# Performance work log

Hardware: AMD Instinct MI355X
Metric: run time of the kernel (lower is better)

Reference implementation:

```python
import jax, jax.numpy as jnp
import numpy as np

S = 72
IMG_W, IMG_H = 640, 360
STRIDE = 32
FMAP_H, FMAP_W = IMG_H // STRIDE, IMG_W // STRIDE  # 11, 20
N_OFFSETS = S
N_STRIPS = S - 1
ANGLES = np.array([15.0, 22.0, 30.0, 39.0, 49.0, 60.0, 72.0, 80.0, 90.0, 100.0, 108.0, 120.0, 131.0, 141.0, 150.0, 158.0, 165.0])
N_ANG = 17
N_PRED = 2 + 2 + 1 + N_OFFSETS  # 77
N_EDGE = FMAP_W + 2 * FMAP_H    # 42
N_PROP = N_ANG * N_EDGE         # 714
NMS_THRES = 15.0
BACKBONE_C = 512
CONV_C = 1024


def _make_anchors():
    anchor_ys = np.linspace(1.0, 0.0, N_OFFSETS)
    tan = np.tan(np.deg2rad(ANGLES))
    def side(origins):
        out = np.zeros((N_ANG, N_PRED, len(origins)), np.float32)
        for i, (sx, sy) in enumerate(origins):
            out[:, 2, i] = 1.0 - sy
            out[:, 3, i] = sx
            out[:, 5:, i] = (sx + (sy - anchor_ys)[None, :] / tan[:, None]) * IMG_W
        return out.reshape(N_ANG * N_PRED, len(origins))
    left = side([(0.0, y) for y in np.linspace(1.0, 0.0, FMAP_H)])
    right = side([(1.0, y) for y in np.linspace(1.0, 0.0, FMAP_H)])
    bottom = side([(x, 1.0) for x in np.linspace(1.0, 0.0, FMAP_W)])
    anchors = np.zeros((N_ANG * N_PRED, FMAP_H, FMAP_W), np.float32)
    anchors[:, :, 0] = left
    anchors[:, :, -1] = right
    anchors[:, -1, :] = bottom
    edge = np.concatenate([anchors[:, :, 0], anchors[:, :, -1], anchors[:, -1, :]], 1)  # [1309,42]
    anch_dim = edge.reshape(N_ANG, N_PRED, N_EDGE).transpose(2, 0, 1).reshape(N_PROP, N_PRED)
    return jnp.asarray(anchors), jnp.asarray(anch_dim)


def setup_inputs():
    key = jax.random.key(0)
    ks = jax.random.split(key, 4)
    B = 32
    feat = jax.random.normal(ks[0], (B, BACKBONE_C, FMAP_H, FMAP_W), jnp.float32)
    W_conv = jax.random.normal(ks[1], (CONV_C, BACKBONE_C), jnp.float32) * 0.02
    b_conv = jnp.zeros((CONV_C,), jnp.float32)
    W_cls = jax.random.normal(ks[2], (2 * N_ANG, CONV_C), jnp.float32) * 0.02
    b_cls = jnp.zeros((2 * N_ANG,), jnp.float32)
    W_reg = jax.random.normal(ks[3], (N_ANG * (N_OFFSETS + 1), CONV_C), jnp.float32) * 0.02
    b_reg = jnp.zeros((N_ANG * (N_OFFSETS + 1),), jnp.float32)
    anchors, anchors_anchor_dim = _make_anchors()
    return {"feat": feat, "W_conv": W_conv, "b_conv": b_conv, "W_cls": W_cls, "b_cls": b_cls,
            "W_reg": W_reg, "b_reg": b_reg, "anchors": anchors, "anchors_anchor_dim": anchors_anchor_dim}


def _proposals(feat, W_conv, b_conv, W_cls, b_cls, W_reg, b_reg, anchors):
    B = feat.shape[0]
    features = jnp.einsum('bchw,oc->bohw', feat, W_conv) + b_conv[None, :, None, None]
    cls_f = jnp.einsum('bchw,oc->bohw', features, W_cls) + b_cls[None, :, None, None]
    reg_f = jnp.einsum('bchw,oc->bohw', features, W_reg) + b_reg[None, :, None, None]
    anch = anchors.reshape(N_ANG, N_PRED, FMAP_H, FMAP_W)
    cls_r = cls_f.reshape(B, N_ANG, 2, FMAP_H, FMAP_W)
    reg_r = reg_f.reshape(B, N_ANG, N_OFFSETS + 1, FMAP_H, FMAP_W)
    # slots 0:2 <- cls logits (set), slots 2:4 <- anchor (copied), slots 4: <- anchor + reg
    mid = jnp.broadcast_to(anch[None, :, 2:4], (B, N_ANG, 2, FMAP_H, FMAP_W))
    tail = anch[None, :, 4:] + reg_r
    lane = jnp.concatenate([cls_r, mid, tail], axis=2)  # [B,17,77,h,w]
    # gather the three feature-map edges: left col, right col, bottom row
    edges = jnp.concatenate([lane[:, :, :, :, 0], lane[:, :, :, :, -1], lane[:, :, :, -1, :]], axis=3)  # [B,17,77,42]
    return edges.transpose(0, 3, 1, 2).reshape(B, N_PROP, N_PRED)  # [B,714,77]


def _nms_one(props, scores):
    # greedy line-NMS over proposals of one image, shapes static
    order = jnp.argsort(-scores)
    p = props[order]
    start = jnp.clip(jnp.round(p[:, 2] * N_STRIPS), 0.0, float(N_STRIPS))
    end = jnp.clip(start + p[:, 4] - 1.0, 0.0, float(N_STRIPS))
    xs = p[:, 5:]  # [N,72]
    s = jnp.maximum(start[:, None], start[None, :])
    e = jnp.minimum(end[:, None], end[None, :])
    idx = jnp.arange(N_OFFSETS, dtype=p.dtype)
    m = (idx[None, None, :] >= s[..., None]) & (idx[None, None, :] <= e[..., None])  # [N,N,72]
    diff = jnp.abs(xs[:, None, :] - xs[None, :, :])  # [N,N,72]
    cnt = e - s + 1.0
    dist = jnp.where(cnt > 0, jnp.sum(diff * m, -1) / jnp.maximum(cnt, 1.0), jnp.inf)
    sup = dist < NMS_THRES
    n = p.shape[0]
    pos = jnp.arange(n)
    def step(suppressed, i):
        keep_i = ~suppressed[i]
        suppressed = suppressed | (keep_i & sup[i] & (pos > i))
        return suppressed, keep_i
    _, keep_sorted = jax.lax.scan(step, jnp.zeros(n, bool), pos)
    return jnp.zeros(n, bool).at[order].set(keep_sorted)


def reference(feat, W_conv, b_conv, W_cls, b_cls, W_reg, b_reg, anchors, anchors_anchor_dim):
    proposals = _proposals(feat, W_conv, b_conv, W_cls, b_cls, W_reg, b_reg, anchors)
    scores = jax.nn.softmax(proposals[..., :2], axis=-1)[..., 1]  # [B,714]
    keep_mask = jax.lax.map(lambda pr: _nms_one(pr[0], pr[1]), (proposals, scores))  # [B,714]
    return proposals, keep_mask, scores
```

## Files before the change

kernel.cpp:

```cpp
#include <hip/hip_runtime.h>
#include <math.h>

#define NB     32
#define FH     11
#define FW     20
#define CIN    512
#define CMID   1024
#define NANG   17
#define NPREDD 77
#define NEDGE  42
#define NPROPP 714
#define NOFF   72
#define NCLS   34
#define NREGR  1241
#define N2PAD  1280
#define MTOT   1344
#define NSTRIPSF 71.0f
#define PADK   40

typedef unsigned long long u64;
typedef unsigned short ushortt;
typedef short s8v __attribute__((ext_vector_type(8)));
typedef ushortt u4v __attribute__((ext_vector_type(4)));
typedef float f4v __attribute__((ext_vector_type(4)));

__device__ inline ushortt f2bf(float f) {
    unsigned u = __float_as_uint(f);
    u += 0x7fffu + ((u >> 16) & 1u);
    return (ushortt)(u >> 16);
}
__device__ inline float bf2f(ushortt h) {
    return __uint_as_float(((unsigned)h) << 16);
}

__global__ __launch_bounds__(256) void k_prep(const float* __restrict__ feat,
                                              ushortt* __restrict__ A1hi,
                                              ushortt* __restrict__ A1lo,
                                              const float* __restrict__ Wconv,
                                              ushortt* __restrict__ B1h,
                                              ushortt* __restrict__ B1l,
                                              const float* __restrict__ Wcls,
                                              const float* __restrict__ Wreg,
                                              ushortt* __restrict__ B2h,
                                              ushortt* __restrict__ B2l)
{
    __shared__ unsigned T[32 * 221];
    int bid = blockIdx.x, tid = threadIdx.x;
    if (bid < 512) {
        int p0 = bid * 32;
        int b  = p0 >> 9;
        int c0 = p0 & 511;
        const float* fp = feat + (size_t)p0 * 220;
        for (int i = tid; i < 32 * 220; i += 256) {
            float v = fp[i];
            int pl = i / 220, off = i - pl * 220;
            ushortt hi = f2bf(v);
            ushortt lo = f2bf(v - bf2f(hi));
            T[pl * 221 + off] = ((unsigned)hi) | (((unsigned)lo) << 16);
        }
        __syncthreads();
        int cl = tid & 31;
        for (int e = tid >> 5; e < NEDGE; e += 8) {
            int hw = (e < FH) ? e * FW
                   : (e < 2 * FH) ? (e - FH) * FW + (FW - 1)
                   : (FH - 1) * FW + (e - 2 * FH);
            unsigned u = T[cl * 221 + hw];
            size_t o = (size_t)(b * NEDGE + e) * CIN + c0 + cl;
            A1hi[o] = (ushortt)(u & 0xffffu);
            A1lo[o] = (ushortt)(u >> 16);
        }
    } else if (bid < 1024) {
        int t = (bid - 512) * 256 + tid;
        float4 v = *(const float4*)(Wconv + (size_t)t * 4);
        float vf[4] = {v.x, v.y, v.z, v.w};
        u4v hv, lv;
#pragma unroll
        for (int j = 0; j < 4; ++j) {
            ushortt h = f2bf(vf[j]);
            hv[j] = h;
            lv[j] = f2bf(vf[j] - bf2f(h));
        }
        *(u4v*)(B1h + (size_t)t * 4) = hv;
        *(u4v*)(B1l + (size_t)t * 4) = lv;
    } else {
        int t = (bid - 1024) * 256 + tid;
        int row = t >> 8, col = (t & 255) * 4;
        float4 v = make_float4(0.f, 0.f, 0.f, 0.f);
        if (row < NCLS)              v = *(const float4*)(Wcls + (size_t)row * CMID + col);
        else if (row < NCLS + NREGR) v = *(const float4*)(Wreg + (size_t)(row - NCLS) * CMID + col);
        float vf[4] = {v.x, v.y, v.z, v.w};
        u4v hv, lv;
#pragma unroll
        for (int j = 0; j < 4; ++j) {
            ushortt h = f2bf(vf[j]);
            hv[j] = h;
            lv[j] = f2bf(vf[j] - bf2f(h));
        }
        *(u4v*)(B2h + (size_t)t * 4) = hv;
        *(u4v*)(B2l + (size_t)t * 4) = lv;
    }
}

#define GEMM_STEP(BUF)                                                               \
    {                                                                                \
        s8v ah[2], al[2], bh[2], bl[2];                                              \
        _Pragma("unroll")                                                            \
        for (int s = 0; s < 2; ++s) {                                                \
            ah[s] = *(const s8v*)&Ash[BUF][(wm + s * 16 + l15) * PADK + quad * 8];   \
            al[s] = *(const s8v*)&Asl[BUF][(wm + s * 16 + l15) * PADK + quad * 8];   \
            bh[s] = *(const s8v*)&Bsh[BUF][(wn + s * 16 + l15) * PADK + quad * 8];   \
            bl[s] = *(const s8v*)&Bsl[BUF][(wn + s * 16 + l15) * PADK + quad * 8];   \
        }                                                                            \
        _Pragma("unroll")                                                            \
        for (int sm = 0; sm < 2; ++sm)                                               \
            _Pragma("unroll")                                                        \
            for (int sn = 0; sn < 2; ++sn) {                                         \
                acc[sm][sn] = __builtin_amdgcn_mfma_f32_16x16x32_bf16(al[sm], bl[sn], acc[sm][sn], 0, 0, 0); \
                acc[sm][sn] = __builtin_amdgcn_mfma_f32_16x16x32_bf16(al[sm], bh[sn], acc[sm][sn], 0, 0, 0); \
                acc[sm][sn] = __builtin_amdgcn_mfma_f32_16x16x32_bf16(ah[sm], bl[sn], acc[sm][sn], 0, 0, 0); \
                acc[sm][sn] = __builtin_amdgcn_mfma_f32_16x16x32_bf16(ah[sm], bh[sn], acc[sm][sn], 0, 0, 0); \
            }                                                                        \
    }

#define LOADSET(dst_a, dst_l, dst_b, dst_c, OFF)                                     \
    dst_a = *(const s8v*)(Ahp + (OFF));                                              \
    dst_l = *(const s8v*)(Alp + (OFF));                                              \
    dst_b = *(const s8v*)(Bhp + (OFF));                                              \
    dst_c = *(const s8v*)(Blp + (OFF));

#define WRITESET(src_a, src_l, src_b, src_c, BUF)                                    \
    *(s8v*)&Ash[BUF][wo] = src_a;                                                    \
    *(s8v*)&Asl[BUF][wo] = src_l;                                                    \
    *(s8v*)&Bsh[BUF][wo] = src_b;                                                    \
    *(s8v*)&Bsl[BUF][wo] = src_c;

__global__ __launch_bounds__(256) void k_gemm1m(const ushortt* __restrict__ Ahi,
                                                const ushortt* __restrict__ Alo,
                                                const ushortt* __restrict__ Bh,
                                                const ushortt* __restrict__ Bl,
                                                const float* __restrict__ bias,
                                                ushortt* __restrict__ Chi,
                                                ushortt* __restrict__ Clo)
{
    const int K = CIN, N = CMID;
    const int NT = K / 32;
    __shared__ __align__(16) ushortt Ash[2][64 * PADK], Asl[2][64 * PADK];
    __shared__ __align__(16) ushortt Bsh[2][64 * PADK], Bsl[2][64 * PADK];
    int tid = threadIdx.x;
    int m0 = blockIdx.y * 64, n0 = blockIdx.x * 64;
    int srow = tid >> 2, sg = tid & 3;
    int lane = tid & 63, wv = tid >> 6;
    int wm = (wv & 1) * 32, wn = (wv >> 1) * 32;
    int quad = lane >> 4, l15 = lane & 15;
    int wo = srow * PADK + sg * 8;

    f4v acc[2][2];
#pragma unroll
    for (int i = 0; i < 2; ++i)
#pragma unroll
        for (int j = 0; j < 2; ++j) acc[i][j] = (f4v){0.f, 0.f, 0.f, 0.f};

    const ushortt* Ahp = Ahi + (size_t)(m0 + srow) * K + sg * 8;
    const ushortt* Alp = Alo + (size_t)(m0 + srow) * K + sg * 8;
    const ushortt* Bhp = Bh  + (size_t)(n0 + srow) * K + sg * 8;
    const ushortt* Blp = Bl  + (size_t)(n0 + srow) * K + sg * 8;

    s8v a0, l0, b0, c0, a1, l1, b1, c1;
    LOADSET(a0, l0, b0, c0, 0)
    WRITESET(a0, l0, b0, c0, 0)
    LOADSET(a1, l1, b1, c1, 32)
    __syncthreads();

    for (int k = 0; k < NT; k += 2) {
        if (k + 2 < NT) { LOADSET(a0, l0, b0, c0, (k + 2) * 32) }
        GEMM_STEP(0)
        WRITESET(a1, l1, b1, c1, 1)
        __syncthreads();
        if (k + 3 < NT) { LOADSET(a1, l1, b1, c1, (k + 3) * 32) }
        GEMM_STEP(1)
        if (k + 2 < NT) { WRITESET(a0, l0, b0, c0, 0) }
        __syncthreads();
    }
#pragma unroll
    for (int sm = 0; sm < 2; ++sm)
#pragma unroll
        for (int sn = 0; sn < 2; ++sn)
#pragma unroll
            for (int r = 0; r < 4; ++r) {
                int m = m0 + wm + sm * 16 + quad * 4 + r;
                int n = n0 + wn + sn * 16 + l15;
                float v = acc[sm][sn][r] + bias[n];
                ushortt h = f2bf(v);
                Chi[(size_t)m * N + n] = h;
                Clo[(size_t)m * N + n] = f2bf(v - bf2f(h));
            }
}

__global__ __launch_bounds__(256) void k_gemm2m(const ushortt* __restrict__ Ahi,
                                                const ushortt* __restrict__ Alo,
                                                const ushortt* __restrict__ Bh,
                                                const ushortt* __restrict__ Bl,
                                                const float* __restrict__ bcls,
                                                const float* __restrict__ breg,
                                                float* __restrict__ C)
{
    const int K = CMID;
    const int NT = K / 32;
    __shared__ __align__(16) ushortt Ash[2][64 * PADK], Asl[2][64 * PADK];
    __shared__ __align__(16) ushortt Bsh[2][64 * PADK], Bsl[2][64 * PADK];
    int tid = threadIdx.x;
    int m0 = blockIdx.y * 64, n0 = blockIdx.x * 64;
    int srow = tid >> 2, sg = tid & 3;
    int lane = tid & 63, wv = tid >> 6;
    int wm = (wv & 1) * 32, wn = (wv >> 1) * 32;
    int quad = lane >> 4, l15 = lane & 15;
    int wo = srow * PADK + sg * 8;

    f4v acc[2][2];
#pragma unroll
    for (int i = 0; i < 2; ++i)
#pragma unroll
        for (int j = 0; j < 2; ++j) acc[i][j] = (f4v){0.f, 0.f, 0.f, 0.f};

    const ushortt* Ahp = Ahi + (size_t)(m0 + srow) * K + sg * 8;
    const ushortt* Alp = Alo + (size_t)(m0 + srow) * K + sg * 8;
    const ushortt* Bhp = Bh  + (size_t)(n0 + srow) * K + sg * 8;
    const ushortt* Blp = Bl  + (size_t)(n0 + srow) * K + sg * 8;

    s8v a0, l0, b0, c0, a1, l1, b1, c1;
    LOADSET(a0, l0, b0, c0, 0)
    WRITESET(a0, l0, b0, c0, 0)
    LOADSET(a1, l1, b1, c1, 32)
    __syncthreads();

    for (int k = 0; k < NT; k += 2) {
        if (k + 2 < NT) { LOADSET(a0, l0, b0, c0, (k + 2) * 32) }
        GEMM_STEP(0)
        WRITESET(a1, l1, b1, c1, 1)
        __syncthreads();
        if (k + 3 < NT) { LOADSET(a1, l1, b1, c1, (k + 3) * 32) }
        GEMM_STEP(1)
        if (k + 2 < NT) { WRITESET(a0, l0, b0, c0, 0) }
        __syncthreads();
    }
#pragma unroll
    for (int sm = 0; sm < 2; ++sm)
#pragma unroll
        for (int sn = 0; sn < 2; ++sn)
#pragma unroll
            for (int r = 0; r < 4; ++r) {
                int m = m0 + wm + sm * 16 + quad * 4 + r;
                int n = n0 + wn + sn * 16 + l15;
                float bb = (n < NCLS) ? bcls[n] : ((n < NCLS + NREGR) ? breg[n - NCLS] : 0.f);
                C[(size_t)m * N2PAD + n] = acc[sm][sn][r] + bb;
            }
}

__global__ __launch_bounds__(256) void k_assemble(const float* __restrict__ C2,
                                                  const float* __restrict__ AD,
                                                  float* __restrict__ outP,
                                                  float* __restrict__ outS,
                                                  float* __restrict__ startv,
                                                  float* __restrict__ endv,
                                                  float* __restrict__ xsel)
{
    int mb = blockIdx.x;
    int b = mb / NEDGE, e = mb - b * NEDGE;
    const float* c2 = C2 + (size_t)mb * N2PAD;
    int tid = threadIdx.x;
    for (int idx = tid; idx < NANG * NPREDD; idx += 256) {
        int a = idx / NPREDD, p = idx - a * NPREDD;
        int prop = e * NANG + a;
        float v;
        if (p < 2) v = c2[a * 2 + p];
        else {
            v = AD[prop * NPREDD + p];
            if (p >= 4) v += c2[NCLS + a * 73 + (p - 4)];
        }
        outP[((size_t)b * NPROPP + prop) * NPREDD + p] = v;
    }
    if (tid < NANG) {
        int a = tid, prop = e * NANG + a;
        float c0 = c2[2 * a], c1 = c2[2 * a + 1];
        float mx = fmaxf(c0, c1);
        float e0 = expf(c0 - mx), e1 = expf(c1 - mx);
        outS[b * NPROPP + prop] = e1 / (e0 + e1);
        float p2 = AD[prop * NPREDD + 2];
        float p4 = AD[prop * NPREDD + 4] + c2[NCLS + a * 73];
        float st = fminf(fmaxf(rintf(p2 * NSTRIPSF), 0.0f), NSTRIPSF);
        float en = fminf(fmaxf(st + p4 - 1.0f, 0.0f), NSTRIPSF);
        startv[b * 720 + prop] = st;
        endv[b * 720 + prop] = en;
        int ksi = (int)st;
        xsel[b * 720 + prop] = AD[prop * NPREDD + 5 + ksi] + c2[NCLS + a * 73 + ksi + 1];
    }
}

__global__ __launch_bounds__(128) void k_sort(const float* __restrict__ scores,
                                              int* __restrict__ order)
{
    int b = blockIdx.x, tile = blockIdx.y, tid = threadIdx.x;
    __shared__ __align__(16) float s[720];
    for (int x = tid; x < 720; x += 128)
        s[x] = (x < NPROPP) ? scores[b * NPROPP + x] : -1e30f;
    __syncthreads();
    int i = tile * 128 + tid;
    if (i >= NPROPP) return;
    float si = s[i];
    int r = 0;
#pragma unroll 4
    for (int j4 = 0; j4 < 720; j4 += 4) {
        float4 v = *(const float4*)&s[j4];
        r += (v.x > si) || (v.x == si && (j4 + 0) < i);
        r += (v.y > si) || (v.y == si && (j4 + 1) < i);
        r += (v.z > si) || (v.z == si && (j4 + 2) < i);
        r += (v.w > si) || (v.w == si && (j4 + 3) < i);
    }
    order[b * 720 + r] = i;
}

__global__ __launch_bounds__(256) void k_supmat(const float* __restrict__ outP,
                                                const float* __restrict__ startv,
                                                const float* __restrict__ endv,
                                                const float* __restrict__ xsel,
                                                const int* __restrict__ order,
                                                u64* __restrict__ sup)
{
    int u = blockIdx.x, b = blockIdx.y;
    int it = 0, rem = 12;
    while (u >= rem) { u -= rem; --rem; ++it; }
    int jt = it + u;
    int i0 = it * 64, j0 = jt * 64;
    int tid = threadIdx.x;
    __shared__ float SI[64], EI[64], XI[64];
    __shared__ float SJ[64], EJ[64], XJ[64];
    __shared__ int   OI[64], OJ[64];
    if (tid < 128) {
        int side = tid >> 6, q = tid & 63;
        int pos = (side ? j0 : i0) + q;
        int o = (pos < NPROPP) ? order[b * 720 + pos] : -1;
        float st = (o >= 0) ? startv[b * 720 + o] : 0.f;
        float en = (o >= 0) ? endv[b * 720 + o] : -2.f;
        float xv = (o >= 0) ? xsel[b * 720 + o] : 0.f;
        if (!side) { SI[q] = st; EI[q] = en; XI[q] = xv; OI[q] = o; }
        else       { SJ[q] = st; EJ[q] = en; XJ[q] = xv; OJ[q] = o; }
    }
    __syncthreads();
    int lane = tid & 63, w = tid >> 6;
    int j = j0 + lane;
    float sj = SJ[lane], ej = EJ[lane], xj = XJ[lane];
    const float* basexs = outP + (size_t)b * NPROPP * NPREDD + 5;
#pragma unroll 1
    for (int rep = 0; rep < 16; ++rep) {
        int iloc = w * 16 + rep;
        int il = i0 + iloc;
        float si = SI[iloc], ei = EI[iloc];
        float s = fmaxf(si, sj), e = fminf(ei, ej);
        float cnt = e - s + 1.0f;
        bool sp = false;
        if (cnt > 0.f) {
            if (e < s) {
                sp = true;
            } else {
                int ks = (int)s, ke = (int)e;
                if (si == sj && ke == ks) {
                    sp = (fabsf(XI[iloc] - xj) / fmaxf(cnt, 1.0f)) < 15.0f;
                } else {
                    const float* xi  = basexs + (size_t)OI[iloc] * NPREDD;
                    const float* xjp = basexs + (size_t)OJ[lane] * NPREDD;
                    float sum = 0.f;
                    for (int k = ks; k <= ke; ++k)
                        sum += fabsf(xi[k] - xjp[k]);
                    sp = (sum / fmaxf(cnt, 1.0f)) < 15.0f;
                }
            }
        }
        bool valid = (il < NPROPP) && (j < NPROPP) && (j > il);
        u64 msk = __ballot(valid && sp);
        if (lane == 0 && il < NPROPP)
            sup[((size_t)b * NPROPP + il) * 12 + jt] = msk;
    }
}

__global__ __launch_bounds__(256) void k_scan(const u64* __restrict__ sup,
                                              const int* __restrict__ order,
                                              float* __restrict__ keep_out)
{
    int b = blockIdx.x, tid = threadIdx.x;
    int lane = tid & 63;
    __shared__ u64 K[12], NS[12];
    __shared__ int changed;
    const u64* base = sup + (size_t)b * NPROPP * 12;

    int r0 = tid, r1 = tid + 256, r2 = tid + 512;
    int t0 = r0 >> 6, t1 = r1 >> 6, t2 = r2 >> 6;
    u64 row0[12], row1[12], row2[12];
#pragma unroll
    for (int t = 0; t < 12; ++t) {
        row0[t] = (t >= t0) ? base[(size_t)r0 * 12 + t] : 0ull;
        row1[t] = (r1 < NPROPP && t >= t1) ? base[(size_t)r1 * 12 + t] : 0ull;
        row2[t] = (r2 < NPROPP && t >= t2) ? base[(size_t)r2 * 12 + t] : 0ull;
    }
    if (tid < 12) {
        K[tid] = (tid < 11) ? ~0ull : ((1ull << (NPROPP - 704)) - 1ull);
        NS[tid] = 0ull;
    }
    __syncthreads();

    for (int sweep = 0; sweep < 720; ++sweep) {
        u64 m0 = 0ull - ((K[r0 >> 6] >> (r0 & 63)) & 1ull);
        u64 m1 = (r1 < NPROPP) ? (0ull - ((K[r1 >> 6] >> (r1 & 63)) & 1ull)) : 0ull;
        u64 m2 = (r2 < NPROPP) ? (0ull - ((K[r2 >> 6] >> (r2 & 63)) & 1ull)) : 0ull;
        unsigned lo[12], hi[12];
#pragma unroll
        for (int t = 0; t < 12; ++t) {
            u64 a = (row0[t] & m0) | (row1[t] & m1) | (row2[t] & m2);
            lo[t] = (unsigned)a;
            hi[t] = (unsigned)(a >> 32);
        }
#pragma unroll
        for (int s = 1; s < 64; s <<= 1) {
#pragma unroll
            for (int t = 0; t < 12; ++t) {
                lo[t] |= __shfl_xor(lo[t], s, 64);
                hi[t] |= __shfl_xor(hi[t], s, 64);
            }
        }
        if (tid == 0) changed = 0;
        if (lane == 0) {
#pragma unroll
            for (int t = 0; t < 12; ++t)
                atomicOr(&NS[t], ((u64)hi[t] << 32) | (u64)lo[t]);
        }
        __syncthreads();
        if (tid < 12) {
            u64 valid = (tid < 11) ? ~0ull : ((1ull << (NPROPP - 704)) - 1ull);
            u64 nk = valid & ~NS[tid];
            if (nk != K[tid]) changed = 1;
            K[tid] = nk;
            NS[tid] = 0ull;
        }
        __syncthreads();
        if (!changed) break;
    }
    if (r0 < NPROPP)
        keep_out[b * NPROPP + order[b * 720 + r0]] =
            ((K[r0 >> 6] >> (r0 & 63)) & 1ull) ? 1.f : 0.f;
    if (r1 < NPROPP)
        keep_out[b * NPROPP + order[b * 720 + r1]] =
            ((K[r1 >> 6] >> (r1 & 63)) & 1ull) ? 1.f : 0.f;
    if (r2 < NPROPP)
        keep_out[b * NPROPP + order[b * 720 + r2]] =
            ((K[r2 >> 6] >> (r2 & 63)) & 1ull) ? 1.f : 0.f;
}

extern "C" void kernel_launch(void* const* d_in, const int* in_sizes, int n_in,
                              void* d_out, int out_size, void* d_ws, size_t ws_size,
                              hipStream_t stream)
{
    const float* feat  = (const float*)d_in[0];
    const float* Wconv = (const float*)d_in[1];
    const float* bconv = (const float*)d_in[2];
    const float* Wcls  = (const float*)d_in[3];
    const float* bcls  = (const float*)d_in[4];
    const float* Wreg  = (const float*)d_in[5];
    const float* breg  = (const float*)d_in[6];
    const float* AD    = (const float*)d_in[8];

    float* out  = (float*)d_out;
    float* outP = out;
    float* outK = out + (size_t)NB * NPROPP * NPREDD;
    float* outS = outK + (size_t)NB * NPROPP;

    float* ws = (float*)d_ws;
    ushortt* A1hi = (ushortt*)ws;
    ushortt* A1lo = (ushortt*)(ws + 344064);
    ushortt* A2hi = (ushortt*)(ws + 688128);
    ushortt* A2lo = (ushortt*)(ws + 1376256);
    float*   C2   = ws + 2064384;
    ushortt* B1h  = (ushortt*)(ws + 3784704);
    ushortt* B1l  = (ushortt*)(ws + 4046848);
    ushortt* B2h  = (ushortt*)(ws + 4308992);
    ushortt* B2l  = (ushortt*)(ws + 4964352);
    float* startv = ws;
    float* endv   = ws + 23040;
    int*   order  = (int*)(ws + 46080);
    u64*   sup    = (u64*)(ws + 69120);
    float* xsel   = ws + 617472;

    k_prep        <<<dim3(2304),       dim3(256), 0, stream>>>(feat, A1hi, A1lo,
                                                               Wconv, B1h, B1l,
                                                               Wcls, Wreg, B2h, B2l);
    k_gemm1m      <<<dim3(16, 21),     dim3(256), 0, stream>>>(A1hi, A1lo, B1h, B1l, bconv, A2hi, A2lo);
    k_gemm2m      <<<dim3(20, 21),     dim3(256), 0, stream>>>(A2hi, A2lo, B2h, B2l, bcls, breg, C2);
    k_assemble    <<<dim3(MTOT),       dim3(256), 0, stream>>>(C2, AD, outP, outS, startv, endv, xsel);
    k_sort        <<<dim3(NB, 6),      dim3(128), 0, stream>>>(outS, order);
    k_supmat      <<<dim3(78, NB),     dim3(256), 0, stream>>>(outP, startv, endv, xsel, order, sup);
    k_scan        <<<dim3(NB),         dim3(256), 0, stream>>>(sup, order, outK);
}
```

Measured before the change: 174.4 us.

## Enlarge GEMM M-tile to 128 rows and skip shuffle reduction in NMS sweep

Both split-bf16 GEMMs now use 128x64 block tiles. Each wave computes a 64x32 sub-tile, so every B fragment loaded from shared memory is reused over four A sub-tiles. A row guard covers the partial last M tile, whose out-of-range A rows are read from neighbouring workspace memory. Fewer blocks are launched, which raises arithmetic intensity but cuts parallelism on a 256-CU part. In the NMS fixed-point scan, a ballot now skips the 6-stage shuffle OR-reduction when a wave has no or few active rows, and those lanes instead atomically OR their words into shared memory directly.

```diff
diff --git a/kernel.cpp b/kernel.cpp
--- a/kernel.cpp
+++ b/kernel.cpp
@@ -103,16 +103,19 @@
 
 #define GEMM_STEP(BUF)                                                               \
     {                                                                                \
-        s8v ah[2], al[2], bh[2], bl[2];                                              \
+        s8v ah[4], al[4], bh[2], bl[2];                                              \
+        _Pragma("unroll")                                                            \
+        for (int s = 0; s < 4; ++s) {                                                \
+            ah[s] = *(const s8v*)&Ash[BUF][(wm + s * 16 + l15) * PADK + quad * 8];   \
+            al[s] = *(const s8v*)&Asl[BUF][(wm + s * 16 + l15) * PADK + quad * 8];   \
+        }                                                                            \
         _Pragma("unroll")                                                            \
         for (int s = 0; s < 2; ++s) {                                                \
-            ah[s] = *(const s8v*)&Ash[BUF][(wm + s * 16 + l15) * PADK + quad * 8];   \
-            al[s] = *(const s8v*)&Asl[BUF][(wm + s * 16 + l15) * PADK + quad * 8];   \
             bh[s] = *(const s8v*)&Bsh[BUF][(wn + s * 16 + l15) * PADK + quad * 8];   \
             bl[s] = *(const s8v*)&Bsl[BUF][(wn + s * 16 + l15) * PADK + quad * 8];   \
         }                                                                            \
         _Pragma("unroll")                                                            \
-        for (int sm = 0; sm < 2; ++sm)                                               \
+        for (int sm = 0; sm < 4; ++sm)                                               \
             _Pragma("unroll")                                                        \
             for (int sn = 0; sn < 2; ++sn) {                                         \
                 acc[sm][sn] = __builtin_amdgcn_mfma_f32_16x16x32_bf16(al[sm], bl[sn], acc[sm][sn], 0, 0, 0); \
@@ -122,17 +125,59 @@
             }                                                                        \
     }
 
-#define LOADSET(dst_a, dst_l, dst_b, dst_c, OFF)                                     \
-    dst_a = *(const s8v*)(Ahp + (OFF));                                              \
-    dst_l = *(const s8v*)(Alp + (OFF));                                              \
-    dst_b = *(const s8v*)(Bhp + (OFF));                                              \
-    dst_c = *(const s8v*)(Blp + (OFF));
-
-#define WRITESET(src_a, src_l, src_b, src_c, BUF)                                    \
-    *(s8v*)&Ash[BUF][wo] = src_a;                                                    \
-    *(s8v*)&Asl[BUF][wo] = src_l;                                                    \
-    *(s8v*)&Bsh[BUF][wo] = src_b;                                                    \
-    *(s8v*)&Bsl[BUF][wo] = src_c;
+#define LOADSET(A, A2, L, L2, Bv, Cv, OFF)                                           \
+    A  = *(const s8v*)(Ahp  + (OFF));                                                \
+    A2 = *(const s8v*)(Ahp2 + (OFF));                                                \
+    L  = *(const s8v*)(Alp  + (OFF));                                                \
+    L2 = *(const s8v*)(Alp2 + (OFF));                                                \
+    Bv = *(const s8v*)(Bhp  + (OFF));                                                \
+    Cv = *(const s8v*)(Blp  + (OFF));
+
+#define WRITESET(A, A2, L, L2, Bv, Cv, BUF)                                          \
+    *(s8v*)&Ash[BUF][wo]  = A;                                                       \
+    *(s8v*)&Ash[BUF][wo2] = A2;                                                      \
+    *(s8v*)&Asl[BUF][wo]  = L;                                                       \
+    *(s8v*)&Asl[BUF][wo2] = L2;                                                      \
+    *(s8v*)&Bsh[BUF][wo]  = Bv;                                                      \
+    *(s8v*)&Bsl[BUF][wo]  = Cv;
+
+#define GEMM_PREAMBLE(Kc)                                                            \
+    int tid = threadIdx.x;                                                           \
+    int m0 = blockIdx.y * 128, n0 = blockIdx.x * 64;                                 \
+    int srow = tid >> 2, sg = tid & 3;                                               \
+    int lane = tid & 63, wv = tid >> 6;                                              \
+    int wm = (wv & 1) * 64, wn = (wv >> 1) * 32;                                     \
+    int quad = lane >> 4, l15 = lane & 15;                                           \
+    int wo = srow * PADK + sg * 8;                                                   \
+    int wo2 = (srow + 64) * PADK + sg * 8;                                           \
+    f4v acc[4][2];                                                                   \
+    _Pragma("unroll")                                                                \
+    for (int i = 0; i < 4; ++i)                                                      \
+        _Pragma("unroll")                                                            \
+        for (int j = 0; j < 2; ++j) acc[i][j] = (f4v){0.f, 0.f, 0.f, 0.f};           \
+    const ushortt* Ahp  = Ahi + (size_t)(m0 + srow) * (Kc) + sg * 8;                 \
+    const ushortt* Ahp2 = Ahp + (size_t)64 * (Kc);                                   \
+    const ushortt* Alp  = Alo + (size_t)(m0 + srow) * (Kc) + sg * 8;                 \
+    const ushortt* Alp2 = Alp + (size_t)64 * (Kc);                                   \
+    const ushortt* Bhp  = Bh  + (size_t)(n0 + srow) * (Kc) + sg * 8;                 \
+    const ushortt* Blp  = Bl  + (size_t)(n0 + srow) * (Kc) + sg * 8;
+
+#define GEMM_MAIN(NT)                                                                \
+    s8v a0, a0b, l0, l0b, b0, c0, a1, a1b, l1, l1b, b1, c1;                          \
+    LOADSET(a0, a0b, l0, l0b, b0, c0, 0)                                             \
+    WRITESET(a0, a0b, l0, l0b, b0, c0, 0)                                            \
+    LOADSET(a1, a1b, l1, l1b, b1, c1, 32)                                            \
+    __syncthreads();                                                                 \
+    for (int k = 0; k < (NT); k += 2) {                                              \
+        if (k + 2 < (NT)) { LOADSET(a0, a0b, l0, l0b, b0, c0, (k + 2) * 32) }        \
+        GEMM_STEP(0)                                                                 \
+        WRITESET(a1, a1b, l1, l1b, b1, c1, 1)                                        \
+        __syncthreads();                                                             \
+        if (k + 3 < (NT)) { LOADSET(a1, a1b, l1, l1b, b1, c1, (k + 3) * 32) }        \
+        GEMM_STEP(1)                                                                 \
+        if (k + 2 < (NT)) { WRITESET(a0, a0b, l0, l0b, b0, c0, 0) }                  \
+        __syncthreads();                                                             \
+    }
 
 __global__ __launch_bounds__(256) void k_gemm1m(const ushortt* __restrict__ Ahi,
                                                 const ushortt* __restrict__ Alo,
@@ -143,56 +188,24 @@
                                                 ushortt* __restrict__ Clo)
 {
     const int K = CIN, N = CMID;
-    const int NT = K / 32;
-    __shared__ __align__(16) ushortt Ash[2][64 * PADK], Asl[2][64 * PADK];
-    __shared__ __align__(16) ushortt Bsh[2][64 * PADK], Bsl[2][64 * PADK];
-    int tid = threadIdx.x;
-    int m0 = blockIdx.y * 64, n0 = blockIdx.x * 64;
-    int srow = tid >> 2, sg = tid & 3;
-    int lane = tid & 63, wv = tid >> 6;
-    int wm = (wv & 1) * 32, wn = (wv >> 1) * 32;
-    int quad = lane >> 4, l15 = lane & 15;
-    int wo = srow * PADK + sg * 8;
-
-    f4v acc[2][2];
-#pragma unroll
-    for (int i = 0; i < 2; ++i)
-#pragma unroll
-        for (int j = 0; j < 2; ++j) acc[i][j] = (f4v){0.f, 0.f, 0.f, 0.f};
-
-    const ushortt* Ahp = Ahi + (size_t)(m0 + srow) * K + sg * 8;
-    const ushortt* Alp = Alo + (size_t)(m0 + srow) * K + sg * 8;
-    const ushortt* Bhp = Bh  + (size_t)(n0 + srow) * K + sg * 8;
-    const ushortt* Blp = Bl  + (size_t)(n0 + srow) * K + sg * 8;
-
-    s8v a0, l0, b0, c0, a1, l1, b1, c1;
-    LOADSET(a0, l0, b0, c0, 0)
-    WRITESET(a0, l0, b0, c0, 0)
-    LOADSET(a1, l1, b1, c1, 32)
-    __syncthreads();
-
-    for (int k = 0; k < NT; k += 2) {
-        if (k + 2 < NT) { LOADSET(a0, l0, b0, c0, (k + 2) * 32) }
-        GEMM_STEP(0)
-        WRITESET(a1, l1, b1, c1, 1)
-        __syncthreads();
-        if (k + 3 < NT) { LOADSET(a1, l1, b1, c1, (k + 3) * 32) }
-        GEMM_STEP(1)
-        if (k + 2 < NT) { WRITESET(a0, l0, b0, c0, 0) }
-        __syncthreads();
-    }
-#pragma unroll
-    for (int sm = 0; sm < 2; ++sm)
+    __shared__ __align__(16) ushortt Ash[2][128 * PADK], Asl[2][128 * PADK];
+    __shared__ __align__(16) ushortt Bsh[2][64 * PADK],  Bsl[2][64 * PADK];
+    GEMM_PREAMBLE(K)
+    GEMM_MAIN(K / 32)
+#pragma unroll
+    for (int sm = 0; sm < 4; ++sm)
 #pragma unroll
         for (int sn = 0; sn < 2; ++sn)
 #pragma unroll
             for (int r = 0; r < 4; ++r) {
                 int m = m0 + wm + sm * 16 + quad * 4 + r;
                 int n = n0 + wn + sn * 16 + l15;
-                float v = acc[sm][sn][r] + bias[n];
-                ushortt h = f2bf(v);
-                Chi[(size_t)m * N + n] = h;
-                Clo[(size_t)m * N + n] = f2bf(v - bf2f(h));
+                if (m < MTOT) {
+                    float v = acc[sm][sn][r] + bias[n];
+                    ushortt h = f2bf(v);
+                    Chi[(size_t)m * N + n] = h;
+                    Clo[(size_t)m * N + n] = f2bf(v - bf2f(h));
+                }
             }
 }
 
@@ -205,54 +218,22 @@
                                                 float* __restrict__ C)
 {
     const int K = CMID;
-    const int NT = K / 32;
-    __shared__ __align__(16) ushortt Ash[2][64 * PADK], Asl[2][64 * PADK];
-    __shared__ __align__(16) ushortt Bsh[2][64 * PADK], Bsl[2][64 * PADK];
-    int tid = threadIdx.x;
-    int m0 = blockIdx.y * 64, n0 = blockIdx.x * 64;
-    int srow = tid >> 2, sg = tid & 3;
-    int lane = tid & 63, wv = tid >> 6;
-    int wm = (wv & 1) * 32, wn = (wv >> 1) * 32;
-    int quad = lane >> 4, l15 = lane & 15;
-    int wo = srow * PADK + sg * 8;
-
-    f4v acc[2][2];
-#pragma unroll
-    for (int i = 0; i < 2; ++i)
-#pragma unroll
-        for (int j = 0; j < 2; ++j) acc[i][j] = (f4v){0.f, 0.f, 0.f, 0.f};
-
-    const ushortt* Ahp = Ahi + (size_t)(m0 + srow) * K + sg * 8;
-    const ushortt* Alp = Alo + (size_t)(m0 + srow) * K + sg * 8;
-    const ushortt* Bhp = Bh  + (size_t)(n0 + srow) * K + sg * 8;
-    const ushortt* Blp = Bl  + (size_t)(n0 + srow) * K + sg * 8;
-
-    s8v a0, l0, b0, c0, a1, l1, b1, c1;
-    LOADSET(a0, l0, b0, c0, 0)
-    WRITESET(a0, l0, b0, c0, 0)
-    LOADSET(a1, l1, b1, c1, 32)
-    __syncthreads();
-
-    for (int k = 0; k < NT; k += 2) {
-        if (k + 2 < NT) { LOADSET(a0, l0, b0, c0, (k + 2) * 32) }
-        GEMM_STEP(0)
-        WRITESET(a1, l1, b1, c1, 1)
-        __syncthreads();
-        if (k + 3 < NT) { LOADSET(a1, l1, b1, c1, (k + 3) * 32) }
-        GEMM_STEP(1)
-        if (k + 2 < NT) { WRITESET(a0, l0, b0, c0, 0) }
-        __syncthreads();
-    }
-#pragma unroll
-    for (int sm = 0; sm < 2; ++sm)
+    __shared__ __align__(16) ushortt Ash[2][128 * PADK], Asl[2][128 * PADK];
+    __shared__ __align__(16) ushortt Bsh[2][64 * PADK],  Bsl[2][64 * PADK];
+    GEMM_PREAMBLE(K)
+    GEMM_MAIN(K / 32)
+#pragma unroll
+    for (int sm = 0; sm < 4; ++sm)
 #pragma unroll
         for (int sn = 0; sn < 2; ++sn)
 #pragma unroll
             for (int r = 0; r < 4; ++r) {
                 int m = m0 + wm + sm * 16 + quad * 4 + r;
                 int n = n0 + wn + sn * 16 + l15;
-                float bb = (n < NCLS) ? bcls[n] : ((n < NCLS + NREGR) ? breg[n - NCLS] : 0.f);
-                C[(size_t)m * N2PAD + n] = acc[sm][sn][r] + bb;
+                if (m < MTOT) {
+                    float bb = (n < NCLS) ? bcls[n] : ((n < NCLS + NREGR) ? breg[n - NCLS] : 0.f);
+                    C[(size_t)m * N2PAD + n] = acc[sm][sn][r] + bb;
+                }
             }
 }
 
@@ -411,26 +392,42 @@
         u64 m0 = 0ull - ((K[r0 >> 6] >> (r0 & 63)) & 1ull);
         u64 m1 = (r1 < NPROPP) ? (0ull - ((K[r1 >> 6] >> (r1 & 63)) & 1ull)) : 0ull;
         u64 m2 = (r2 < NPROPP) ? (0ull - ((K[r2 >> 6] >> (r2 & 63)) & 1ull)) : 0ull;
-        unsigned lo[12], hi[12];
+        u64 a[12], any = 0ull;
 #pragma unroll
         for (int t = 0; t < 12; ++t) {
-            u64 a = (row0[t] & m0) | (row1[t] & m1) | (row2[t] & m2);
-            lo[t] = (unsigned)a;
-            hi[t] = (unsigned)(a >> 32);
-        }
-#pragma unroll
-        for (int s = 1; s < 64; s <<= 1) {
-#pragma unroll
-            for (int t = 0; t < 12; ++t) {
-                lo[t] |= __shfl_xor(lo[t], s, 64);
-                hi[t] |= __shfl_xor(hi[t], s, 64);
+            a[t] = (row0[t] & m0) | (row1[t] & m1) | (row2[t] & m2);
+            any |= a[t];
+        }
+        if (tid == 0) changed = 0;
+        u64 act = __ballot(any != 0ull);
+        if (act) {
+            if (__popcll(act) > 24) {
+                unsigned lo[12], hi[12];
+#pragma unroll
+                for (int t = 0; t < 12; ++t) {
+                    lo[t] = (unsigned)a[t];
+                    hi[t] = (unsigned)(a[t] >> 32);
+                }
+#pragma unroll
+                for (int s = 1; s < 64; s <<= 1) {
+#pragma unroll
+                    for (int t = 0; t < 12; ++t) {
+                        lo[t] |= __shfl_xor(lo[t], s, 64);
+                        hi[t] |= __shfl_xor(hi[t], s, 64);
+                    }
+                }
+                if (lane == 0) {
+#pragma unroll
+                    for (int t = 0; t < 12; ++t) {
+                        u64 w = ((u64)hi[t] << 32) | (u64)lo[t];
+                        if (w) atomicOr(&NS[t], w);
+                    }
+                }
+            } else if (any) {
+#pragma unroll
+                for (int t = 0; t < 12; ++t)
+                    if (a[t]) atomicOr(&NS[t], a[t]);
             }
-        }
-        if (tid == 0) changed = 0;
-        if (lane == 0) {
-#pragma unroll
-            for (int t = 0; t < 12; ++t)
-                atomicOr(&NS[t], ((u64)hi[t] << 32) | (u64)lo[t]);
         }
         __syncthreads();
         if (tid < 12) {
@@ -491,8 +488,8 @@
     k_prep        <<<dim3(2304),       dim3(256), 0, stream>>>(feat, A1hi, A1lo,
                                                                Wconv, B1h, B1l,
                                                                Wcls, Wreg, B2h, B2l);
-    k_gemm1m      <<<dim3(16, 21),     dim3(256), 0, stream>>>(A1hi, A1lo, B1h, B1l, bconv, A2hi, A2lo);
-    k_gemm2m      <<<dim3(20, 21),     dim3(256), 0, stream>>>(A2hi, A2lo, B2h, B2l, bcls, breg, C2);
+    k_gemm1m      <<<dim3(16, 11),     dim3(256), 0, stream>>>(A1hi, A1lo, B1h, B1l, bconv, A2hi, A2lo);
+    k_gemm2m      <<<dim3(20, 11),     dim3(256), 0, stream>>>(A2hi, A2lo, B2h, B2l, bcls, breg, C2);
     k_assemble    <<<dim3(MTOT),       dim3(256), 0, stream>>>(C2, AD, outP, outS, startv, endv, xsel);
     k_sort        <<<dim3(NB, 6),      dim3(128), 0, stream>>>(outS, order);
     k_supmat      <<<dim3(78, NB),     dim3(256), 0, stream>>>(outP, startv, endv, xsel, order, sup);
```

Result: slower. 191.1 us (+9.6%).
